# Kernel tuning notes

Hardware: AMD Instinct MI355X
Metric: run time of the kernel (lower is better)

Reference implementation:

```python
import jax, jax.numpy as jnp
import numpy as np
import math

DIM_IN = 512
DIM_OUT = 512
KERNEL = 3
STYLE_DIM = 2 * 128
LIN_SCALE = 1.0 / math.sqrt(STYLE_DIM)      # EqualLinear scale (lr_mul=1)
CONV_SCALE = 1.0 / math.sqrt(DIM_IN * KERNEL ** 2)  # fan_in = dim_in * k**2 (as in source)
PAD = KERNEL // 2


def setup_inputs() -> dict:
    key = jax.random.key(0)
    ks = jax.random.split(key, 5)
    B, T = 16, 2048
    x = jax.random.normal(ks[0], (B, DIM_IN, T), dtype=jnp.float32)
    c_src = jax.random.normal(ks[1], (B, 128), dtype=jnp.float32)
    c_trg = jax.random.normal(ks[2], (B, 128), dtype=jnp.float32)
    style_w = jax.random.normal(ks[3], (DIM_IN, STYLE_DIM), dtype=jnp.float32)
    style_b = jnp.ones((DIM_IN,), dtype=jnp.float32)  # bias_init=1
    weight = jax.random.normal(ks[4], (1, DIM_OUT, DIM_IN, KERNEL), dtype=jnp.float32)
    return {"x": x, "c_src": c_src, "c_trg": c_trg,
            "style_w": style_w, "style_b": style_b, "weight": weight}


def reference(x, c_src, c_trg, style_w, style_b, weight):
    B = x.shape[0]
    # EqualLinear: style code s [B, dim_in]
    c = jnp.concatenate([c_src, c_trg], axis=-1)              # [B, 256]
    s = c @ (style_w * LIN_SCALE).T + style_b                 # [B, dim_in]
    # Modulate: w [B, dim_out, dim_in, k]
    w = CONV_SCALE * weight * s[:, None, :, None]
    # Demodulate over (dim_in, k)
    demod = jax.lax.rsqrt(jnp.sum(w * w, axis=(2, 3)) + 1e-8)  # [B, dim_out]
    w = w * demod[:, :, None, None]
    # Per-sample conv1d, padding 'same' (pad = k//2), vmapped over batch
    def conv1(xi, wi):
        # xi: [dim_in, T], wi: [dim_out, dim_in, k]
        out = jax.lax.conv_general_dilated(
            xi[None], wi, window_strides=(1,), padding=[(PAD, PAD)],
            dimension_numbers=("NCH", "OIH", "NCH"))
        return out[0]                                          # [dim_out, T]
    return jax.vmap(conv1)(x, w)                               # [B, dim_out, T]
```

## Files before the change

kernel.cpp:

```cpp
#include <hip/hip_runtime.h>
#include <cstdint>
#include <cstddef>


#define LIN_SCALE  0.0625f
#define CONV_SCALE 0.014731391f

#define B_   16
#define CIN  512
#define COUT 512
#define T_   2048
#define TP   2050

typedef __bf16 bf16x8 __attribute__((ext_vector_type(8)));
typedef float  f32x4  __attribute__((ext_vector_type(4)));
typedef unsigned short u16x8 __attribute__((ext_vector_type(8)));
typedef unsigned short u16x2 __attribute__((ext_vector_type(2)));

__device__ inline unsigned short f2bf(float f) {
  __bf16 h = (__bf16)f;
  return __builtin_bit_cast(unsigned short, h);
}

__global__ __launch_bounds__(256) void style_kernel(const float* __restrict__ c_src,
                                                    const float* __restrict__ c_trg,
                                                    const float* __restrict__ sw,
                                                    const float* __restrict__ sb,
                                                    float* __restrict__ s) {
  __shared__ float c[256];
  const int b = blockIdx.y;
  const int tid = threadIdx.x;
  c[tid] = (tid < 128) ? c_src[b * 128 + tid] : c_trg[b * 128 + tid - 128];
  __syncthreads();
  const int w = tid >> 6, lane = tid & 63;
  #pragma unroll
  for (int rr = 0; rr < 16; ++rr) {
    const int i = blockIdx.x * 64 + w * 16 + rr;
    const float* row = sw + (size_t)i * 256;
    float acc = row[lane] * c[lane] + row[lane + 64] * c[lane + 64]
              + row[lane + 128] * c[lane + 128] + row[lane + 192] * c[lane + 192];
    #pragma unroll
    for (int off = 32; off; off >>= 1) acc += __shfl_down(acc, off, 64);
    if (lane == 0) s[b * 512 + i] = acc * LIN_SCALE + sb[i];
  }
}

__global__ __launch_bounds__(256) void modw_kernel(const float* __restrict__ weight,
                                                   const float* __restrict__ s,
                                                   unsigned short* __restrict__ Wm) {
  const int o = blockIdx.x;
  const int tid = threadIdx.x;
  __shared__ float wsh[1536];
  __shared__ float svs[16 * 512];
  __shared__ float partial[16][4];
  __shared__ float demv[16];

  #pragma unroll
  for (int j = tid; j < 1536; j += 256) wsh[j] = weight[(size_t)o * 1536 + j];
  #pragma unroll
  for (int j = tid; j < 16 * 512; j += 256) svs[j] = s[j];
  __syncthreads();

  float wr[6];
  #pragma unroll
  for (int q = 0; q < 6; ++q) wr[q] = wsh[tid * 6 + q] * CONV_SCALE;

  const int lane = tid & 63, w = tid >> 6;
  float ssb[16];
  #pragma unroll
  for (int b = 0; b < 16; ++b) {
    const float s0 = svs[b * 512 + 2 * tid];
    const float s1 = svs[b * 512 + 2 * tid + 1];
    float ss = 0.f;
    #pragma unroll
    for (int q = 0; q < 3; ++q) { float v = wr[q] * s0;     ss += v * v; }
    #pragma unroll
    for (int q = 3; q < 6; ++q) { float v = wr[q] * s1;     ss += v * v; }
    ssb[b] = ss;
  }
  #pragma unroll
  for (int b = 0; b < 16; ++b) {
    float ss = ssb[b];
    #pragma unroll
    for (int off = 32; off; off >>= 1) ss += __shfl_down(ss, off, 64);
    if (lane == 0) partial[b][w] = ss;
  }
  __syncthreads();
  if (tid < 16)
    demv[tid] = rsqrtf(partial[tid][0] + partial[tid][1] + partial[tid][2] + partial[tid][3] + 1e-8f);
  __syncthreads();

  #pragma unroll
  for (int b = 0; b < 16; ++b) {
    const float dem = demv[b];
    const float s0 = svs[b * 512 + 2 * tid] * dem;
    const float s1 = svs[b * 512 + 2 * tid + 1] * dem;
    #pragma unroll
    for (int k = 0; k < 3; ++k) {
      u16x2 v;
      v.x = f2bf(wr[k] * s0);
      v.y = f2bf(wr[3 + k] * s1);
      *(u16x2*)&Wm[(((size_t)b * 3 + k) * 512 + o) * 512 + 2 * tid] = v;
    }
  }
}

__global__ __launch_bounds__(256) void transpose_kernel(const float* __restrict__ x,
                                                        unsigned short* __restrict__ xT) {
  __shared__ float tile[64][65];
  const int b = blockIdx.z, i0 = blockIdx.y * 64, t0 = blockIdx.x * 64;
  const int tid = threadIdx.x;

  const int lr = tid >> 4;
  const int lc = (tid & 15) * 4;
  const float* xb = x + ((size_t)b * CIN + i0) * T_ + t0;
  #pragma unroll
  for (int p = 0; p < 4; ++p) {
    const int r = p * 16 + lr;
    const float4 v = *(const float4*)(xb + (size_t)r * T_ + lc);
    tile[r][lc + 0] = v.x; tile[r][lc + 1] = v.y;
    tile[r][lc + 2] = v.z; tile[r][lc + 3] = v.w;
  }
  __syncthreads();

  const int st = tid >> 3;
  const int si = (tid & 7) * 8;
  unsigned short* xTb = xT + ((size_t)b * TP + 1 + t0) * CIN + i0;
  #pragma unroll
  for (int p = 0; p < 2; ++p) {
    const int t = p * 32 + st;
    u16x8 v;
    #pragma unroll
    for (int q = 0; q < 8; ++q) v[q] = f2bf(tile[si + q][t]);
    *(u16x8*)&xTb[(size_t)t * CIN + si] = v;
  }
}

__global__ void zpad_kernel(unsigned short* __restrict__ xT) {
  const int b = blockIdx.x;
  const size_t base = (size_t)b * TP * CIN;
  for (int j = threadIdx.x; j < CIN; j += 256) {
    xT[base + j] = 0;
    xT[base + (size_t)(TP - 1) * CIN + j] = 0;
  }
}

#define BM 128
#define BN 128
#define BK 64

__global__ __launch_bounds__(256, 4) void gemm_kernel(const unsigned short* __restrict__ Wm,
                                                      const unsigned short* __restrict__ xT,
                                                      float* __restrict__ out) {
  __shared__ unsigned short lA[BM * BK];
  __shared__ unsigned short lB[BN * BK];

  const int b  = blockIdx.z;
  const int o0 = blockIdx.y * BM;
  const int t0 = blockIdx.x * BN;
  const int tid  = threadIdx.x;
  const int lane = tid & 63;
  const int wm = (threadIdx.x >> 6 & 1) * 64;
  const int wn = (threadIdx.x >> 7) * 64;

  const int srow = tid >> 3;
  const int scol = (tid & 7) * 8;
  const unsigned short* gW = Wm + (size_t)b * 3 * 512 * 512 + (size_t)(o0 + srow) * 512 + scol;
  const unsigned short* gX = xT + (size_t)b * TP * CIN + (size_t)(t0 + srow) * CIN + scol;
  unsigned short* lAp = &lA[tid * 8];
  unsigned short* lBp = &lB[tid * 8];

  f32x4 acc[4][4];
  #pragma unroll
  for (int i = 0; i < 4; ++i)
    #pragma unroll
    for (int j = 0; j < 4; ++j) acc[i][j] = (f32x4){0.f, 0.f, 0.f, 0.f};

  for (int kk = 0; kk < 24; ++kk) {
    const int tap = kk >> 3;
    const int i0  = (kk & 7) * 64;
    const size_t offA = (size_t)tap * 512 * 512 + i0;
    const size_t offX = (size_t)tap * CIN + i0;
    __syncthreads();
    #pragma unroll
    for (int p = 0; p < 4; ++p)
      __builtin_amdgcn_global_load_lds(
          (const __attribute__((address_space(1))) void*)(gW + offA + (size_t)p * 32 * 512),
          (__attribute__((address_space(3))) void*)(lAp + p * 2048), 16, 0, 0);
    #pragma unroll
    for (int p = 0; p < 4; ++p)
      __builtin_amdgcn_global_load_lds(
          (const __attribute__((address_space(1))) void*)(gX + offX + (size_t)p * 32 * CIN),
          (__attribute__((address_space(3))) void*)(lBp + p * 2048), 16, 0, 0);
    __syncthreads();

    #pragma unroll
    for (int s = 0; s < 2; ++s) {
      const int ko = s * 32 + (lane >> 4) * 8;
      bf16x8 af[4], bfr[4];
      #pragma unroll
      for (int mi = 0; mi < 4; ++mi)
        af[mi] = *(const bf16x8*)&lA[(wm + mi * 16 + (lane & 15)) * BK + ko];
      #pragma unroll
      for (int ni = 0; ni < 4; ++ni)
        bfr[ni] = *(const bf16x8*)&lB[(wn + ni * 16 + (lane & 15)) * BK + ko];
      #pragma unroll
      for (int mi = 0; mi < 4; ++mi)
        #pragma unroll
        for (int ni = 0; ni < 4; ++ni)
          acc[mi][ni] = __builtin_amdgcn_mfma_f32_16x16x32_bf16(af[mi], bfr[ni], acc[mi][ni], 0, 0, 0);
    }
  }

  float* ob = out + ((size_t)b * COUT + o0 + wm) * T_ + t0 + wn;
  const int rrow = (lane >> 4) * 4;
  const int ccol = lane & 15;
  #pragma unroll
  for (int mi = 0; mi < 4; ++mi)
    #pragma unroll
    for (int ni = 0; ni < 4; ++ni)
      #pragma unroll
      for (int r = 0; r < 4; ++r)
        ob[(size_t)(mi * 16 + rrow + r) * T_ + ni * 16 + ccol] = acc[mi][ni][r];
}

extern "C" void kernel_launch(void* const* d_in, const int* in_sizes, int n_in,
                              void* d_out, int out_size, void* d_ws, size_t ws_size,
                              hipStream_t stream) {
  const float* x       = (const float*)d_in[0];
  const float* c_src   = (const float*)d_in[1];
  const float* c_trg   = (const float*)d_in[2];
  const float* style_w = (const float*)d_in[3];
  const float* style_b = (const float*)d_in[4];
  const float* weight  = (const float*)d_in[5];
  float* out = (float*)d_out;

  char* ws = (char*)d_ws;
  float* s_buf          = (float*)ws;
  unsigned short* Wm    = (unsigned short*)(ws + 32768);
  unsigned short* xTbuf = (unsigned short*)(ws + 32768 + 25165824);

  style_kernel<<<dim3(8, 16), 256, 0, stream>>>(c_src, c_trg, style_w, style_b, s_buf);
  modw_kernel<<<dim3(COUT), 256, 0, stream>>>(weight, s_buf, Wm);
  transpose_kernel<<<dim3(T_ / 64, CIN / 64, B_), 256, 0, stream>>>(x, xTbuf);
  zpad_kernel<<<dim3(B_), 256, 0, stream>>>(xTbuf);
  gemm_kernel<<<dim3(T_ / BN, COUT / BM, B_), 256, 0, stream>>>(Wm, xTbuf, out);
}
```

Measured before the change: 212.4 us.

## Reuse shared X tile across three conv taps with swizzled LDS and XCD-aware mapping

The GEMM now loads one 258-row X tile per K-chunk and reads it at offsets 0..2 for the three taps, instead of reloading X separately for each tap. Tiles change to 64x256 with all three tap weight slices held in LDS, and an XOR swizzle on LDS columns avoids bank conflicts. Blocks are remapped so each XCD handles whole batches, which should improve L2 locality. The zero-padding kernel is folded into the transpose kernel, removing one launch; in exchange LDS use rises and occupancy falls to two blocks per CU.

Result: faster. 188.9 us (-11.0%).

```diff
diff --git a/kernel.cpp b/kernel.cpp
--- a/kernel.cpp
+++ b/kernel.cpp
@@ -73,9 +73,9 @@
     const float s1 = svs[b * 512 + 2 * tid + 1];
     float ss = 0.f;
     #pragma unroll
-    for (int q = 0; q < 3; ++q) { float v = wr[q] * s0;     ss += v * v; }
-    #pragma unroll
-    for (int q = 3; q < 6; ++q) { float v = wr[q] * s1;     ss += v * v; }
+    for (int q = 0; q < 3; ++q) { float v = wr[q] * s0; ss += v * v; }
+    #pragma unroll
+    for (int q = 3; q < 6; ++q) { float v = wr[q] * s1; ss += v * v; }
     ssb[b] = ss;
   }
   #pragma unroll
@@ -121,6 +121,10 @@
     tile[r][lc + 0] = v.x; tile[r][lc + 1] = v.y;
     tile[r][lc + 2] = v.z; tile[r][lc + 3] = v.w;
   }
+  if (blockIdx.x == 0 && tid < 8)
+    *(u16x8*)&xT[(size_t)b * TP * CIN + i0 + tid * 8] = (u16x8){0,0,0,0,0,0,0,0};
+  if (blockIdx.x == gridDim.x - 1 && tid < 8)
+    *(u16x8*)&xT[((size_t)b * TP + TP - 1) * CIN + i0 + tid * 8] = (u16x8){0,0,0,0,0,0,0,0};
   __syncthreads();
 
   const int st = tid >> 3;
@@ -136,83 +140,92 @@
   }
 }
 
-__global__ void zpad_kernel(unsigned short* __restrict__ xT) {
-  const int b = blockIdx.x;
-  const size_t base = (size_t)b * TP * CIN;
-  for (int j = threadIdx.x; j < CIN; j += 256) {
-    xT[base + j] = 0;
-    xT[base + (size_t)(TP - 1) * CIN + j] = 0;
-  }
-}
-
-#define BM 128
-#define BN 128
+#define BM 64
+#define BN 256
 #define BK 64
 
-__global__ __launch_bounds__(256, 4) void gemm_kernel(const unsigned short* __restrict__ Wm,
+__global__ __launch_bounds__(256, 2) void gemm_kernel(const unsigned short* __restrict__ Wm,
                                                       const unsigned short* __restrict__ xT,
                                                       float* __restrict__ out) {
-  __shared__ unsigned short lA[BM * BK];
-  __shared__ unsigned short lB[BN * BK];
-
-  const int b  = blockIdx.z;
-  const int o0 = blockIdx.y * BM;
-  const int t0 = blockIdx.x * BN;
+  __shared__ unsigned short lA[3 * 64 * 64];
+  __shared__ unsigned short lB[258 * 64];
+
+  const int id  = blockIdx.x;
+  const int xcd = id & 7;
+  const int j   = id >> 3;
+  const int b   = xcd + 8 * (j >> 6);
+  const int r   = j & 63;
+  const int o0  = (r >> 3) * BM;
+  const int t0  = (r & 7) * BN;
+
   const int tid  = threadIdx.x;
   const int lane = tid & 63;
-  const int wm = (threadIdx.x >> 6 & 1) * 64;
-  const int wn = (threadIdx.x >> 7) * 64;
-
-  const int srow = tid >> 3;
-  const int scol = (tid & 7) * 8;
-  const unsigned short* gW = Wm + (size_t)b * 3 * 512 * 512 + (size_t)(o0 + srow) * 512 + scol;
-  const unsigned short* gX = xT + (size_t)b * TP * CIN + (size_t)(t0 + srow) * CIN + scol;
-  unsigned short* lAp = &lA[tid * 8];
-  unsigned short* lBp = &lB[tid * 8];
+  const int wn   = (tid >> 6) * 64;
+
+  const int srow  = tid >> 3;
+  const int sxcol = ((tid & 7) ^ (srow & 7)) * 8;
+  const unsigned short* gW = Wm + ((size_t)b * 3 * 512 + o0) * 512;
+  const unsigned short* gX = xT + ((size_t)b * TP + t0) * CIN;
 
   f32x4 acc[4][4];
   #pragma unroll
   for (int i = 0; i < 4; ++i)
     #pragma unroll
-    for (int j = 0; j < 4; ++j) acc[i][j] = (f32x4){0.f, 0.f, 0.f, 0.f};
-
-  for (int kk = 0; kk < 24; ++kk) {
-    const int tap = kk >> 3;
-    const int i0  = (kk & 7) * 64;
-    const size_t offA = (size_t)tap * 512 * 512 + i0;
-    const size_t offX = (size_t)tap * CIN + i0;
+    for (int jj = 0; jj < 4; ++jj) acc[i][jj] = (f32x4){0.f, 0.f, 0.f, 0.f};
+
+  for (int kk = 0; kk < 8; ++kk) {
+    const int i0 = kk * 64;
     __syncthreads();
     #pragma unroll
-    for (int p = 0; p < 4; ++p)
+    for (int tap = 0; tap < 3; ++tap)
+      #pragma unroll
+      for (int p = 0; p < 2; ++p)
+        __builtin_amdgcn_global_load_lds(
+            (const __attribute__((address_space(1))) void*)
+              (gW + (size_t)tap * 512 * 512 + (size_t)(p * 32 + srow) * 512 + i0 + sxcol),
+            (__attribute__((address_space(3))) void*)(&lA[tap * 4096 + p * 2048 + tid * 8]),
+            16, 0, 0);
+    #pragma unroll
+    for (int q = 0; q < 8; ++q)
       __builtin_amdgcn_global_load_lds(
-          (const __attribute__((address_space(1))) void*)(gW + offA + (size_t)p * 32 * 512),
-          (__attribute__((address_space(3))) void*)(lAp + p * 2048), 16, 0, 0);
-    #pragma unroll
-    for (int p = 0; p < 4; ++p)
+          (const __attribute__((address_space(1))) void*)
+            (gX + (size_t)(q * 32 + srow) * CIN + i0 + sxcol),
+          (__attribute__((address_space(3))) void*)(&lB[(q * 256 + tid) * 8]),
+          16, 0, 0);
+    if (tid < 16)
       __builtin_amdgcn_global_load_lds(
-          (const __attribute__((address_space(1))) void*)(gX + offX + (size_t)p * 32 * CIN),
-          (__attribute__((address_space(3))) void*)(lBp + p * 2048), 16, 0, 0);
+          (const __attribute__((address_space(1))) void*)
+            (gX + (size_t)(256 + srow) * CIN + i0 + sxcol),
+          (__attribute__((address_space(3))) void*)(&lB[(2048 + tid) * 8]),
+          16, 0, 0);
     __syncthreads();
 
     #pragma unroll
-    for (int s = 0; s < 2; ++s) {
-      const int ko = s * 32 + (lane >> 4) * 8;
-      bf16x8 af[4], bfr[4];
+    for (int k = 0; k < 3; ++k) {
       #pragma unroll
-      for (int mi = 0; mi < 4; ++mi)
-        af[mi] = *(const bf16x8*)&lA[(wm + mi * 16 + (lane & 15)) * BK + ko];
-      #pragma unroll
-      for (int ni = 0; ni < 4; ++ni)
-        bfr[ni] = *(const bf16x8*)&lB[(wn + ni * 16 + (lane & 15)) * BK + ko];
-      #pragma unroll
-      for (int mi = 0; mi < 4; ++mi)
+      for (int s = 0; s < 2; ++s) {
+        const int kc = s * 4 + (lane >> 4);
+        bf16x8 af[4], bfr[4];
         #pragma unroll
-        for (int ni = 0; ni < 4; ++ni)
-          acc[mi][ni] = __builtin_amdgcn_mfma_f32_16x16x32_bf16(af[mi], bfr[ni], acc[mi][ni], 0, 0, 0);
+        for (int mi = 0; mi < 4; ++mi) {
+          const int ra = mi * 16 + (lane & 15);
+          af[mi] = *(const bf16x8*)&lA[k * 4096 + ra * 64 + ((kc ^ (ra & 7)) << 3)];
+        }
+        #pragma unroll
+        for (int ni = 0; ni < 4; ++ni) {
+          const int rb = wn + ni * 16 + (lane & 15) + k;
+          bfr[ni] = *(const bf16x8*)&lB[rb * 64 + ((kc ^ (rb & 7)) << 3)];
+        }
+        #pragma unroll
+        for (int mi = 0; mi < 4; ++mi)
+          #pragma unroll
+          for (int ni = 0; ni < 4; ++ni)
+            acc[mi][ni] = __builtin_amdgcn_mfma_f32_16x16x32_bf16(af[mi], bfr[ni], acc[mi][ni], 0, 0, 0);
+      }
     }
   }
 
-  float* ob = out + ((size_t)b * COUT + o0 + wm) * T_ + t0 + wn;
+  float* ob = out + ((size_t)b * COUT + o0) * T_ + t0 + wn;
   const int rrow = (lane >> 4) * 4;
   const int ccol = lane & 15;
   #pragma unroll
@@ -220,8 +233,8 @@
     #pragma unroll
     for (int ni = 0; ni < 4; ++ni)
       #pragma unroll
-      for (int r = 0; r < 4; ++r)
-        ob[(size_t)(mi * 16 + rrow + r) * T_ + ni * 16 + ccol] = acc[mi][ni][r];
+      for (int rr = 0; rr < 4; ++rr)
+        ob[(size_t)(mi * 16 + rrow + rr) * T_ + ni * 16 + ccol] = acc[mi][ni][rr];
 }
 
 extern "C" void kernel_launch(void* const* d_in, const int* in_sizes, int n_in,
@@ -243,6 +256,5 @@
   style_kernel<<<dim3(8, 16), 256, 0, stream>>>(c_src, c_trg, style_w, style_b, s_buf);
   modw_kernel<<<dim3(COUT), 256, 0, stream>>>(weight, s_buf, Wm);
   transpose_kernel<<<dim3(T_ / 64, CIN / 64, B_), 256, 0, stream>>>(x, xTbuf);
-  zpad_kernel<<<dim3(B_), 256, 0, stream>>>(xTbuf);
-  gemm_kernel<<<dim3(T_ / BN, COUT / BM, B_), 256, 0, stream>>>(Wm, xTbuf, out);
-}
+  gemm_kernel<<<dim3(1024), 256, 0, stream>>>(Wm, xTbuf, out);
+}
```
